# Kernel optimization log

Hardware: AMD Instinct MI355X
Metric: run time of the kernel (lower is better)

## Reference

```python
import jax, jax.numpy as jnp
import numpy as np

VOCAB = 32000
N = 4096        # reservoir_size
D = 32          # avg nonzeros per row -> density D/N
R_OUT = 512
BATCH = 8
T = 256
NNZ = N * D     # W_rec nonzeros = N*N*(D/N)


def setup_inputs() -> dict:
    key = jax.random.key(0)
    ks = jax.random.split(key, 9)
    x = jax.random.randint(ks[0], (BATCH, T), 0, VOCAB)
    # dense input table; sparse.mm(W_in_T, one_hot) == row gather W_in[x_t]
    W_in = jax.random.normal(ks[1], (VOCAB, N), jnp.float32)
    rec_rows = jax.random.randint(ks[2], (NNZ,), 0, N, dtype=jnp.int32)
    rec_cols = jax.random.randint(ks[3], (NNZ,), 0, N, dtype=jnp.int32)
    # small scale stands in for spectral-radius normalization (init-time detail)
    rec_vals = jax.random.normal(ks[4], (NNZ,), jnp.float32) * 0.05
    a = jax.random.uniform(ks[5], (N,), jnp.float32)  # leak rates in [0,1)
    B_w = jax.random.normal(ks[6], (R_OUT, N), jnp.float32) / np.sqrt(N)
    A_w = jax.random.normal(ks[7], (VOCAB, R_OUT), jnp.float32) / np.sqrt(R_OUT)
    A_b = jnp.zeros((VOCAB,), jnp.float32)
    return dict(x=x, W_in=W_in, rec_rows=rec_rows, rec_cols=rec_cols,
                rec_vals=rec_vals, a=a, B_w=B_w, A_w=A_w, A_b=A_b)


def reference(x, W_in, rec_rows, rec_cols, rec_vals, a, B_w, A_w, A_b):
    B = x.shape[0]

    def step(h, x_t):
        # input projection: one-hot @ W_in  ==  row gather
        u = W_in[x_t]                                   # (B, N)
        # sparse COO matvec: rec = W_rec @ h^T, batched over B
        contrib = rec_vals[None, :] * h[:, rec_cols]    # (B, nnz)
        rec = jnp.zeros_like(h).at[:, rec_rows].add(contrib)
        pre = jnp.clip(u + rec, -10.0, 10.0)
        h_new = (1.0 - a) * h + a * jnp.tanh(pre)
        out = (h_new @ B_w.T) @ A_w.T + A_b             # (B, vocab)
        return h_new, out

    h0 = jnp.zeros((B, W_in.shape[1]), W_in.dtype)
    _, outs = jax.lax.scan(step, h0, x.T)               # (T, B, V)
    return jnp.transpose(outs, (1, 0, 2))               # (B, T, V)
```

## Files before the change

kernel.cpp:

```cpp
#include <hip/hip_runtime.h>
#include <hip/hip_bf16.h>
#include <stdint.h>

#define N_RES 4096
#define BATCH 8
#define T_STEPS 256
#define VOCAB 32000
#define R_OUT 512
#define NNZ 131072
#define NNZ_CAP 163840
#define TEAMS 8
#define SLICES 16
#define ROWS_PS 256
#define NWG (TEAMS*SLICES)
#define CSR_CAP 10240

typedef _Float16 v8h __attribute__((ext_vector_type(8)));
typedef float v4f __attribute__((ext_vector_type(4)));

static __device__ __forceinline__ unsigned short f2h(float f) {
    _Float16 h = (_Float16)f;
    unsigned short u;
    __builtin_memcpy(&u, &h, 2);
    return u;
}
static __device__ __forceinline__ float h2f(unsigned short u) {
    _Float16 h;
    __builtin_memcpy(&h, &u, 2);
    return (float)h;
}


#define FLAG_WORDS (TEAMS * SLICES * 32)
#define INIT_WORDS (NNZ_CAP + 4096 + FLAG_WORDS)

__global__ __launch_bounds__(256) void k_init(unsigned* __restrict__ csr,
                                              int* __restrict__ cnt,
                                              unsigned* __restrict__ flags) {
    int i = blockIdx.x * 256 + threadIdx.x;
    if (i < NNZ_CAP) csr[i] = 0u;
    else if (i < NNZ_CAP + 4096) cnt[i - NNZ_CAP] = 0;
    else if (i < INIT_WORDS) flags[i - NNZ_CAP - 4096] = 0u;
}


__global__ __launch_bounds__(256) void k_hist(const int* __restrict__ rows,
                                              int* __restrict__ cnt) {
    int i = blockIdx.x * 256 + threadIdx.x;
    if (i < NNZ) atomicAdd(&cnt[rows[i]], 1);
}

__global__ __launch_bounds__(1024) void k_scan(const int* __restrict__ cnt,
                                               int* __restrict__ row_ptr,
                                               int* __restrict__ cursor) {
    __shared__ int sm[1024];
    int t = threadIdx.x;
    int base = t * 4;
    int c0 = (cnt[base] + 7) & ~7;
    int c1 = (cnt[base + 1] + 7) & ~7;
    int c2 = (cnt[base + 2] + 7) & ~7;
    int c3 = (cnt[base + 3] + 7) & ~7;
    int s = c0 + c1 + c2 + c3;
    sm[t] = s;
    __syncthreads();
    for (int off = 1; off < 1024; off <<= 1) {
        int v = (t >= off) ? sm[t - off] : 0;
        __syncthreads();
        sm[t] += v;
        __syncthreads();
    }
    int run = sm[t] - s;
    row_ptr[base] = run;     cursor[base] = run;     run += c0;
    row_ptr[base + 1] = run; cursor[base + 1] = run; run += c1;
    row_ptr[base + 2] = run; cursor[base + 2] = run; run += c2;
    row_ptr[base + 3] = run; cursor[base + 3] = run; run += c3;
    if (t == 1023) row_ptr[4096] = run;
}

__global__ __launch_bounds__(256) void k_fill(const int* __restrict__ rows,
                                              const int* __restrict__ cols,
                                              const float* __restrict__ vals,
                                              int* __restrict__ cursor,
                                              unsigned* __restrict__ csr) {
    int i = blockIdx.x * 256 + threadIdx.x;
    if (i < NNZ) {
        int r = rows[i];
        int c = cols[i];
        int p = atomicAdd(&cursor[r], 1);
        unsigned off = ((unsigned)(c & 15) << 10) | ((unsigned)(c >> 4) << 2);
        csr[p] = (off << 16) | (unsigned)f2h(vals[i]);
    }
}


#define NB8 (R_OUT * N_RES / 8)
#define NA8 (VOCAB * R_OUT / 8)

__global__ __launch_bounds__(256) void k_cvt2(const float* __restrict__ Bw,
                                              unsigned short* __restrict__ Bwh,
                                              const float* __restrict__ Aw,
                                              unsigned short* __restrict__ Awh) {
    int i = blockIdx.x * 256 + threadIdx.x;
    const float* src;
    unsigned short* dst;
    int j;
    if (i < NB8) { src = Bw; dst = Bwh; j = i * 8; }
    else if (i < NB8 + NA8) { src = Aw; dst = Awh; j = (i - NB8) * 8; }
    else return;
    float4 a0 = *reinterpret_cast<const float4*>(src + j);
    float4 a1 = *reinterpret_cast<const float4*>(src + j + 4);
    unsigned short o[8] = { f2h(a0.x), f2h(a0.y), f2h(a0.z), f2h(a0.w),
                            f2h(a1.x), f2h(a1.y), f2h(a1.z), f2h(a1.w) };
    *reinterpret_cast<uint4*>(dst + j) = *reinterpret_cast<const uint4*>(o);
}


__global__ __launch_bounds__(256) void k_steps(const int* __restrict__ rowptr,
                                               const unsigned* __restrict__ csr,
                                               const float* __restrict__ W_in,
                                               const int* __restrict__ x,
                                               const float* __restrict__ a,
                                               unsigned short* __restrict__ Hb,
                                               unsigned* __restrict__ hx,
                                               unsigned* __restrict__ flags) {
    __shared__ float plane[4096];
    __shared__ __align__(16) unsigned lcsr[CSR_CAP];
    __shared__ int ltok[T_STEPS];

    int wg = blockIdx.x;
    int tid = threadIdx.x;
    int team = wg & 7;
    int slice = wg >> 3;
    int r_own = slice * ROWS_PS + tid;

    ltok[tid] = x[team * T_STEPS + tid];

    int j0 = rowptr[slice * ROWS_PS];
    int j1 = rowptr[slice * ROWS_PS + ROWS_PS];
    int cntE = j1 - j0;
    if (cntE > CSR_CAP) cntE = CSR_CAP;
    {
        const uint4* src = reinterpret_cast<const uint4*>(csr + j0);
        int n4 = cntE >> 2;
        for (int k = tid; k < n4; k += 256)
            reinterpret_cast<uint4*>(lcsr)[k] = src[k];
    }
    for (int k = tid; k < 4096; k += 256) plane[k] = 0.f;

    int js = rowptr[r_own] - j0;
    int je = rowptr[r_own + 1] - j0;
    if (js > CSR_CAP) js = CSR_CAP;
    if (je > CSR_CAP) je = CSR_CAP;
    float av = a[r_own];
    float oma = 1.f - av;
    int pown = ((r_own & 15) << 8) | (r_own >> 4);
    __syncthreads();

    float u_cur = W_in[(size_t)ltok[0] * N_RES + r_own];

    for (int t = 0; t < T_STEPS; ++t) {
        float u_nxt = 0.f;
        if (t + 1 < T_STEPS)
            u_nxt = W_in[(size_t)ltok[t + 1] * N_RES + r_own];

        float acc = 0.f;
        for (int j = js; j < je; j += 8) {
            uint4 e0 = *reinterpret_cast<const uint4*>(lcsr + j);
            uint4 e1 = *reinterpret_cast<const uint4*>(lcsr + j + 4);
            unsigned ee[8] = { e0.x, e0.y, e0.z, e0.w, e1.x, e1.y, e1.z, e1.w };
#pragma unroll
            for (int q = 0; q < 8; ++q) {
                float g = *reinterpret_cast<const float*>(
                    reinterpret_cast<const char*>(plane) + (ee[q] >> 16));
                acc += h2f((unsigned short)(ee[q] & 0xffffu)) * g;
            }
        }
        float hold = plane[pown];
        float pre = u_cur + acc;
        pre = fminf(fmaxf(pre, -10.f), 10.f);
        float ex = __expf(2.f * pre);
        float th = 1.f - 2.f / (ex + 1.f);
        float hv = oma * hold + av * th;
        unsigned short hv16 = f2h(hv);

        if (t == T_STEPS - 1) {
            Hb[((size_t)(team * T_STEPS + t) << 12) + r_own] = hv16;
            break;
        }

        unsigned e = (unsigned)(t + 1);
        unsigned* xb = hx + (((size_t)(e & 1u) * TEAMS + team) << 12);

        __hip_atomic_store(xb + r_own, (e << 16) | (unsigned)hv16,
                           __ATOMIC_RELAXED, __HIP_MEMORY_SCOPE_AGENT);
        __syncthreads();
        if (tid == 0)
            __hip_atomic_store(flags + (team * SLICES + slice) * 32, e,
                               __ATOMIC_RELAXED, __HIP_MEMORY_SCOPE_AGENT);

        Hb[((size_t)(team * T_STEPS + t) << 12) + r_own] = hv16;

        if (tid < SLICES) {
            const unsigned* fp = flags + (team * SLICES + tid) * 32;
            while (__hip_atomic_load(fp, __ATOMIC_RELAXED,
                                     __HIP_MEMORY_SCOPE_AGENT) < e) {}
        }
        __syncthreads();

        uint4 v0, v1, v2, v3;
        const char* p0 = reinterpret_cast<const char*>(xb) + (size_t)tid * 16;
        const char* p1 = p0 + 4096;
        const char* p2 = p0 + 8192;
        const char* p3 = p0 + 12288;
        asm volatile(
            "global_load_dwordx4 %0, %4, off sc0 sc1\n\t"
            "global_load_dwordx4 %1, %5, off sc0 sc1\n\t"
            "global_load_dwordx4 %2, %6, off sc0 sc1\n\t"
            "global_load_dwordx4 %3, %7, off sc0 sc1\n\t"
            "s_waitcnt vmcnt(0)"
            : "=&v"(v0), "=&v"(v1), "=&v"(v2), "=&v"(v3)
            : "v"(p0), "v"(p1), "v"(p2), "v"(p3)
            : "memory");
#define QOK(v) (((v.x >> 16) == e) && ((v.y >> 16) == e) && \
                ((v.z >> 16) == e) && ((v.w >> 16) == e))
        int tries = 0;
        while (!(QOK(v0) && QOK(v1) && QOK(v2) && QOK(v3)) && tries <= 64) {
            ++tries;
            if (!QOK(v0)) asm volatile("global_load_dwordx4 %0, %1, off sc0 sc1\n\ts_waitcnt vmcnt(0)" : "=&v"(v0) : "v"(p0) : "memory");
            if (!QOK(v1)) asm volatile("global_load_dwordx4 %0, %1, off sc0 sc1\n\ts_waitcnt vmcnt(0)" : "=&v"(v1) : "v"(p1) : "memory");
            if (!QOK(v2)) asm volatile("global_load_dwordx4 %0, %1, off sc0 sc1\n\ts_waitcnt vmcnt(0)" : "=&v"(v2) : "v"(p2) : "memory");
            if (!QOK(v3)) asm volatile("global_load_dwordx4 %0, %1, off sc0 sc1\n\ts_waitcnt vmcnt(0)" : "=&v"(v3) : "v"(p3) : "memory");
        }
        if (tries > 64) {
            unsigned w[16];
#pragma unroll
            for (int k = 0; k < 16; ++k) {
                const unsigned* wp = xb + (k >> 2) * 1024 + tid * 4 + (k & 3);
                unsigned g = __hip_atomic_load(wp, __ATOMIC_RELAXED, __HIP_MEMORY_SCOPE_AGENT);
                while ((g >> 16) != e)
                    g = __hip_atomic_load(wp, __ATOMIC_RELAXED, __HIP_MEMORY_SCOPE_AGENT);
                w[k] = g;
            }
            v0 = (uint4){w[0], w[1], w[2], w[3]};
            v1 = (uint4){w[4], w[5], w[6], w[7]};
            v2 = (uint4){w[8], w[9], w[10], w[11]};
            v3 = (uint4){w[12], w[13], w[14], w[15]};
        }
#undef QOK
        {
            unsigned wv[16] = { v0.x, v0.y, v0.z, v0.w, v1.x, v1.y, v1.z, v1.w,
                                v2.x, v2.y, v2.z, v2.w, v3.x, v3.y, v3.z, v3.w };
#pragma unroll
            for (int q = 0; q < 4; ++q)
#pragma unroll
                for (int i = 0; i < 4; ++i) {
                    int r = (q << 10) + 4 * tid + i;
                    plane[((r & 15) << 8) | (r >> 4)] =
                        h2f((unsigned short)(wv[q * 4 + i] & 0xffffu));
                }
        }
        u_cur = u_nxt;
        __syncthreads();
    }
}


static __device__ __forceinline__ void stage128x32(const _Float16* __restrict__ g,
                                                   int ld, int row0, int k0,
                                                   _Float16* lds, int wave, int lane) {
#pragma unroll
    for (int q = 0; q < 2; ++q) {
        int i = wave * 128 + q * 64 + lane;
        const _Float16* src = g + (size_t)(row0 + (i >> 2)) * ld + k0 + (i & 3) * 8;
        int loff = __builtin_amdgcn_readfirstlane((wave * 128 + q * 64) * 16);
        __builtin_amdgcn_global_load_lds(
            (const __attribute__((address_space(1))) void*)src,
            (__attribute__((address_space(3))) void*)((char*)lds + loff),
            16, 0, 0);
    }
}

static __device__ __forceinline__ void stage64x32(const _Float16* __restrict__ g,
                                                  int ld, int row0, int k0,
                                                  _Float16* lds, int wave, int lane) {
    int i = wave * 64 + lane;
    const _Float16* src = g + (size_t)(row0 + (i >> 2)) * ld + k0 + (i & 3) * 8;
    int loff = __builtin_amdgcn_readfirstlane(wave * 64 * 16);
    __builtin_amdgcn_global_load_lds(
        (const __attribute__((address_space(1))) void*)src,
        (__attribute__((address_space(3))) void*)((char*)lds + loff),
        16, 0, 0);
}


__global__ __launch_bounds__(256) void k_gemm1(const _Float16* __restrict__ Hb,
                                               const _Float16* __restrict__ Bwh,
                                               unsigned short* __restrict__ Rbh) {
    __shared__ _Float16 As[2][64 * 32];
    __shared__ _Float16 Bs[2][64 * 32];
    int tid = threadIdx.x, lane = tid & 63, wave = tid >> 6;
    int wm = wave >> 1, wn = wave & 1;
    int col0 = blockIdx.x * 64;
    int row0 = blockIdx.y * 64;
    int rA = lane & 15, kA = (lane >> 4) * 8;
    v4f acc[2][2];
#pragma unroll
    for (int s = 0; s < 2; ++s)
#pragma unroll
        for (int f = 0; f < 2; ++f) acc[s][f] = (v4f){0.f, 0.f, 0.f, 0.f};

    stage64x32(Hb,  N_RES, row0, 0, As[0], wave, lane);
    stage64x32(Bwh, N_RES, col0, 0, Bs[0], wave, lane);
    const int NIT = N_RES / 32;
    for (int it = 0; it < NIT; ++it) {
        int cur = it & 1;
        __syncthreads();
        asm volatile("s_waitcnt vmcnt(0)" ::: "memory");
        __syncthreads();
        if (it + 1 < NIT) {
            stage64x32(Hb,  N_RES, row0, (it + 1) * 32, As[cur ^ 1], wave, lane);
            stage64x32(Bwh, N_RES, col0, (it + 1) * 32, Bs[cur ^ 1], wave, lane);
        }
        v8h af[2], bf[2];
#pragma unroll
        for (int s = 0; s < 2; ++s)
            af[s] = *reinterpret_cast<const v8h*>(&As[cur][(wm * 32 + s * 16 + rA) * 32 + kA]);
#pragma unroll
        for (int f = 0; f < 2; ++f)
            bf[f] = *reinterpret_cast<const v8h*>(&Bs[cur][(wn * 32 + f * 16 + rA) * 32 + kA]);
#pragma unroll
        for (int s = 0; s < 2; ++s)
#pragma unroll
            for (int f = 0; f < 2; ++f)
                acc[s][f] = __builtin_amdgcn_mfma_f32_16x16x32_f16(af[s], bf[f], acc[s][f], 0, 0, 0);
    }
#pragma unroll
    for (int f = 0; f < 2; ++f) {
        int col = col0 + wn * 32 + f * 16 + (lane & 15);
#pragma unroll
        for (int s = 0; s < 2; ++s)
#pragma unroll
            for (int r = 0; r < 2 * 2; ++r) {
                int row = row0 + wm * 32 + s * 16 + (lane >> 4) * 4 + r;
                Rbh[(size_t)row * R_OUT + col] = f2h(acc[s][f][r]);
            }
    }
}


__global__ __launch_bounds__(256) void k_gemm2(const _Float16* __restrict__ Rbh,
                                               const _Float16* __restrict__ Awh,
                                               const float* __restrict__ Ab,
                                               float* __restrict__ out) {
    __shared__ _Float16 As[2][128 * 32];
    __shared__ _Float16 Bs[2][128 * 32];
    int tid = threadIdx.x, lane = tid & 63, wave = tid >> 6;
    int wm = wave >> 1, wn = wave & 1;
    int col0 = blockIdx.x * 128;
    int row0 = blockIdx.y * 128;
    int rA = lane & 15, kA = (lane >> 4) * 8;
    v4f acc[4][4];
#pragma unroll
    for (int s = 0; s < 4; ++s)
#pragma unroll
        for (int f = 0; f < 4; ++f) acc[s][f] = (v4f){0.f, 0.f, 0.f, 0.f};

    stage128x32(Rbh, R_OUT, row0, 0, As[0], wave, lane);
    stage128x32(Awh, R_OUT, col0, 0, Bs[0], wave, lane);
    const int NIT = R_OUT / 32;
    for (int it = 0; it < NIT; ++it) {
        int cur = it & 1;
        __syncthreads();
        asm volatile("s_waitcnt vmcnt(0)" ::: "memory");
        __syncthreads();
        if (it + 1 < NIT) {
            stage128x32(Rbh, R_OUT, row0, (it + 1) * 32, As[cur ^ 1], wave, lane);
            stage128x32(Awh, R_OUT, col0, (it + 1) * 32, Bs[cur ^ 1], wave, lane);
        }
        v8h af[4], bf[4];
#pragma unroll
        for (int s = 0; s < 4; ++s)
            af[s] = *reinterpret_cast<const v8h*>(&As[cur][(wm * 64 + s * 16 + rA) * 32 + kA]);
#pragma unroll
        for (int f = 0; f < 4; ++f)
            bf[f] = *reinterpret_cast<const v8h*>(&Bs[cur][(wn * 64 + f * 16 + rA) * 32 + kA]);
#pragma unroll
        for (int s = 0; s < 4; ++s)
#pragma unroll
            for (int f = 0; f < 4; ++f)
                acc[s][f] = __builtin_amdgcn_mfma_f32_16x16x32_f16(af[s], bf[f], acc[s][f], 0, 0, 0);
    }
#pragma unroll
    for (int f = 0; f < 4; ++f) {
        float bias = Ab[col0 + wn * 64 + f * 16 + (lane & 15)];
#pragma unroll
        for (int s = 0; s < 4; ++s)
#pragma unroll
            for (int r = 0; r < 4; ++r) acc[s][f][r] += bias;
    }
    float* Ct = (float*)As;
#pragma unroll
    for (int s = 0; s < 4; ++s) {
        __syncthreads();
#pragma unroll
        for (int f = 0; f < 4; ++f) {
            int lc = wn * 64 + f * 16 + (lane & 15);
            int lr = wm * 16 + (lane >> 4) * 4;
#pragma unroll
            for (int r = 0; r < 4; ++r)
                Ct[(lr + r) * 128 + lc] = acc[s][f][r];
        }
        __syncthreads();
        int lr2 = tid >> 3;
        int lc2 = (tid & 7) * 16;
        int grow = row0 + (lr2 & 15) + (lr2 >> 4) * 64 + s * 16;
        float* dst = out + (size_t)grow * VOCAB + col0 + lc2;
        const float* srcl = &Ct[lr2 * 128 + lc2];
#pragma unroll
        for (int v = 0; v < 4; ++v)
            *reinterpret_cast<float4*>(dst + v * 4) =
                *reinterpret_cast<const float4*>(srcl + v * 4);
    }
}


extern "C" void kernel_launch(void* const* d_in, const int* in_sizes, int n_in,
                              void* d_out, int out_size, void* d_ws, size_t ws_size,
                              hipStream_t stream) {
    const int*   x        = (const int*)d_in[0];
    const float* W_in     = (const float*)d_in[1];
    const int*   rec_rows = (const int*)d_in[2];
    const int*   rec_cols = (const int*)d_in[3];
    const float* rec_vals = (const float*)d_in[4];
    const float* a        = (const float*)d_in[5];
    const float* B_w      = (const float*)d_in[6];
    const float* A_w      = (const float*)d_in[7];
    const float* A_b      = (const float*)d_in[8];
    float* out = (float*)d_out;

    char* w = (char*)d_ws;
    size_t off = 0;
    auto alloc = [&](size_t bytes) { void* p = w + off; off = (off + bytes + 255) & ~(size_t)255; return p; };

    unsigned short* Hb     = (unsigned short*)alloc((size_t)2048 * N_RES * 2);
    unsigned short* Rbh    = (unsigned short*)alloc((size_t)2048 * R_OUT * 2);
    unsigned short* Bwh    = (unsigned short*)alloc((size_t)R_OUT * N_RES * 2);
    unsigned short* Awh    = (unsigned short*)alloc((size_t)VOCAB * R_OUT * 2);
    unsigned*       csr    = (unsigned*)alloc((size_t)NNZ_CAP * 4);
    int*            rowptr = (int*)alloc(4097 * 4);
    int*            cnt    = (int*)alloc(4096 * 4);
    int*            cursor = (int*)alloc(4096 * 4);
    unsigned*       hx     = (unsigned*)alloc((size_t)2 * TEAMS * 4096 * 4);
    unsigned*       flags  = (unsigned*)alloc(FLAG_WORDS * 4);

    k_init<<<(INIT_WORDS + 255) / 256, 256, 0, stream>>>(csr, cnt, flags);

    k_hist<<<(NNZ + 255) / 256, 256, 0, stream>>>(rec_rows, cnt);
    k_scan<<<1, 1024, 0, stream>>>(cnt, rowptr, cursor);
    k_fill<<<(NNZ + 255) / 256, 256, 0, stream>>>(rec_rows, rec_cols, rec_vals, cursor, csr);

    k_cvt2<<<(NB8 + NA8 + 255) / 256, 256, 0, stream>>>(B_w, Bwh, A_w, Awh);

    k_steps<<<NWG, 256, 0, stream>>>(rowptr, csr, W_in, x, a, Hb, hx, flags);

    k_gemm1<<<dim3(R_OUT / 64, 2048 / 64), 256, 0, stream>>>(
        (const _Float16*)Hb, (const _Float16*)Bwh, Rbh);
    k_gemm2<<<dim3(VOCAB / 128, 2048 / 128), 256, 0, stream>>>(
        (const _Float16*)Rbh, (const _Float16*)Awh, A_b, out);
}
```

Baseline: 1.280 ms.

## Use linear h plane layout, deepen gemm2 K tile, add nontemporal output stores

The recurrent step kernel drops the permuted (r&15,r>>4) plane layout for a linear one. CSR column offsets are now plain byte offsets, and the per-step plane refill becomes four vectorized float4 LDS stores instead of sixteen scattered scalar writes. The output GEMM stages 64-wide K tiles (two 32-wide halves) per iteration, halving the number of barriers and waits, and it writes the large logits output with nontemporal stores. hx is also zeroed in init. A linear layout can bring back LDS bank conflicts on the random gathers, and the larger LDS footprint may reduce gemm2 occupancy.

```diff
diff --git a/kernel.cpp b/kernel.cpp
--- a/kernel.cpp
+++ b/kernel.cpp
@@ -32,15 +32,18 @@
 
 
 #define FLAG_WORDS (TEAMS * SLICES * 32)
-#define INIT_WORDS (NNZ_CAP + 4096 + FLAG_WORDS)
+#define HX_WORDS   (2 * TEAMS * 4096)
+#define INIT_WORDS (NNZ_CAP + 4096 + FLAG_WORDS + HX_WORDS)
 
 __global__ __launch_bounds__(256) void k_init(unsigned* __restrict__ csr,
                                               int* __restrict__ cnt,
-                                              unsigned* __restrict__ flags) {
+                                              unsigned* __restrict__ flags,
+                                              unsigned* __restrict__ hx) {
     int i = blockIdx.x * 256 + threadIdx.x;
     if (i < NNZ_CAP) csr[i] = 0u;
     else if (i < NNZ_CAP + 4096) cnt[i - NNZ_CAP] = 0;
-    else if (i < INIT_WORDS) flags[i - NNZ_CAP - 4096] = 0u;
+    else if (i < NNZ_CAP + 4096 + FLAG_WORDS) flags[i - NNZ_CAP - 4096] = 0u;
+    else if (i < INIT_WORDS) hx[i - NNZ_CAP - 4096 - FLAG_WORDS] = 0u;
 }
 
 
@@ -85,9 +88,8 @@
     int i = blockIdx.x * 256 + threadIdx.x;
     if (i < NNZ) {
         int r = rows[i];
-        int c = cols[i];
+        unsigned off = (unsigned)(cols[i] << 2);
         int p = atomicAdd(&cursor[r], 1);
-        unsigned off = ((unsigned)(c & 15) << 10) | ((unsigned)(c >> 4) << 2);
         csr[p] = (off << 16) | (unsigned)f2h(vals[i]);
     }
 }
@@ -153,7 +155,6 @@
     if (je > CSR_CAP) je = CSR_CAP;
     float av = a[r_own];
     float oma = 1.f - av;
-    int pown = ((r_own & 15) << 8) | (r_own >> 4);
     __syncthreads();
 
     float u_cur = W_in[(size_t)ltok[0] * N_RES + r_own];
@@ -175,7 +176,7 @@
                 acc += h2f((unsigned short)(ee[q] & 0xffffu)) * g;
             }
         }
-        float hold = plane[pown];
+        float hold = plane[r_own];
         float pre = u_cur + acc;
         pre = fminf(fmaxf(pre, -10.f), 10.f);
         float ex = __expf(2.f * pre);
@@ -248,16 +249,16 @@
         }
 #undef QOK
         {
-            unsigned wv[16] = { v0.x, v0.y, v0.z, v0.w, v1.x, v1.y, v1.z, v1.w,
-                                v2.x, v2.y, v2.z, v2.w, v3.x, v3.y, v3.z, v3.w };
-#pragma unroll
-            for (int q = 0; q < 4; ++q)
-#pragma unroll
-                for (int i = 0; i < 4; ++i) {
-                    int r = (q << 10) + 4 * tid + i;
-                    plane[((r & 15) << 8) | (r >> 4)] =
-                        h2f((unsigned short)(wv[q * 4 + i] & 0xffffu));
-                }
+            uint4 qs[4] = { v0, v1, v2, v3 };
+#pragma unroll
+            for (int q = 0; q < 4; ++q) {
+                v4f fv;
+                fv.x = h2f((unsigned short)(qs[q].x & 0xffffu));
+                fv.y = h2f((unsigned short)(qs[q].y & 0xffffu));
+                fv.z = h2f((unsigned short)(qs[q].z & 0xffffu));
+                fv.w = h2f((unsigned short)(qs[q].w & 0xffffu));
+                *reinterpret_cast<v4f*>(&plane[(q << 10) + 4 * tid]) = fv;
+            }
         }
         u_cur = u_nxt;
         __syncthreads();
@@ -340,7 +341,7 @@
 #pragma unroll
         for (int s = 0; s < 2; ++s)
 #pragma unroll
-            for (int r = 0; r < 2 * 2; ++r) {
+            for (int r = 0; r < 4; ++r) {
                 int row = row0 + wm * 32 + s * 16 + (lane >> 4) * 4 + r;
                 Rbh[(size_t)row * R_OUT + col] = f2h(acc[s][f][r]);
             }
@@ -352,8 +353,8 @@
                                                const _Float16* __restrict__ Awh,
                                                const float* __restrict__ Ab,
                                                float* __restrict__ out) {
-    __shared__ _Float16 As[2][128 * 32];
-    __shared__ _Float16 Bs[2][128 * 32];
+    __shared__ _Float16 As[2][128 * 64];
+    __shared__ _Float16 Bs[2][128 * 64];
     int tid = threadIdx.x, lane = tid & 63, wave = tid >> 6;
     int wm = wave >> 1, wn = wave & 1;
     int col0 = blockIdx.x * 128;
@@ -365,30 +366,40 @@
 #pragma unroll
         for (int f = 0; f < 4; ++f) acc[s][f] = (v4f){0.f, 0.f, 0.f, 0.f};
 
-    stage128x32(Rbh, R_OUT, row0, 0, As[0], wave, lane);
-    stage128x32(Awh, R_OUT, col0, 0, Bs[0], wave, lane);
-    const int NIT = R_OUT / 32;
+    stage128x32(Rbh, R_OUT, row0, 0,  As[0], wave, lane);
+    stage128x32(Rbh, R_OUT, row0, 32, As[0] + 128 * 32, wave, lane);
+    stage128x32(Awh, R_OUT, col0, 0,  Bs[0], wave, lane);
+    stage128x32(Awh, R_OUT, col0, 32, Bs[0] + 128 * 32, wave, lane);
+    const int NIT = R_OUT / 64;
     for (int it = 0; it < NIT; ++it) {
         int cur = it & 1;
         __syncthreads();
         asm volatile("s_waitcnt vmcnt(0)" ::: "memory");
         __syncthreads();
         if (it + 1 < NIT) {
-            stage128x32(Rbh, R_OUT, row0, (it + 1) * 32, As[cur ^ 1], wave, lane);
-            stage128x32(Awh, R_OUT, col0, (it + 1) * 32, Bs[cur ^ 1], wave, lane);
-        }
-        v8h af[4], bf[4];
-#pragma unroll
-        for (int s = 0; s < 4; ++s)
-            af[s] = *reinterpret_cast<const v8h*>(&As[cur][(wm * 64 + s * 16 + rA) * 32 + kA]);
-#pragma unroll
-        for (int f = 0; f < 4; ++f)
-            bf[f] = *reinterpret_cast<const v8h*>(&Bs[cur][(wn * 64 + f * 16 + rA) * 32 + kA]);
-#pragma unroll
-        for (int s = 0; s < 4; ++s)
+            int k0 = (it + 1) * 64;
+            stage128x32(Rbh, R_OUT, row0, k0,      As[cur ^ 1], wave, lane);
+            stage128x32(Rbh, R_OUT, row0, k0 + 32, As[cur ^ 1] + 128 * 32, wave, lane);
+            stage128x32(Awh, R_OUT, col0, k0,      Bs[cur ^ 1], wave, lane);
+            stage128x32(Awh, R_OUT, col0, k0 + 32, Bs[cur ^ 1] + 128 * 32, wave, lane);
+        }
+#pragma unroll
+        for (int ks = 0; ks < 2; ++ks) {
+            const _Float16* ab = &As[cur][ks * 128 * 32];
+            const _Float16* bb = &Bs[cur][ks * 128 * 32];
+            v8h af[4], bf[4];
+#pragma unroll
+            for (int s = 0; s < 4; ++s)
+                af[s] = *reinterpret_cast<const v8h*>(&ab[(wm * 64 + s * 16 + rA) * 32 + kA]);
 #pragma unroll
             for (int f = 0; f < 4; ++f)
-                acc[s][f] = __builtin_amdgcn_mfma_f32_16x16x32_f16(af[s], bf[f], acc[s][f], 0, 0, 0);
+                bf[f] = *reinterpret_cast<const v8h*>(&bb[(wn * 64 + f * 16 + rA) * 32 + kA]);
+#pragma unroll
+            for (int s = 0; s < 4; ++s)
+#pragma unroll
+                for (int f = 0; f < 4; ++f)
+                    acc[s][f] = __builtin_amdgcn_mfma_f32_16x16x32_f16(af[s], bf[f], acc[s][f], 0, 0, 0);
+        }
     }
 #pragma unroll
     for (int f = 0; f < 4; ++f) {
@@ -418,8 +429,9 @@
         const float* srcl = &Ct[lr2 * 128 + lc2];
 #pragma unroll
         for (int v = 0; v < 4; ++v)
-            *reinterpret_cast<float4*>(dst + v * 4) =
-                *reinterpret_cast<const float4*>(srcl + v * 4);
+            __builtin_nontemporal_store(
+                *reinterpret_cast<const v4f*>(srcl + v * 4),
+                reinterpret_cast<v4f*>(dst + v * 4));
     }
 }
 
@@ -450,10 +462,10 @@
     int*            rowptr = (int*)alloc(4097 * 4);
     int*            cnt    = (int*)alloc(4096 * 4);
     int*            cursor = (int*)alloc(4096 * 4);
-    unsigned*       hx     = (unsigned*)alloc((size_t)2 * TEAMS * 4096 * 4);
+    unsigned*       hx     = (unsigned*)alloc((size_t)HX_WORDS * 4);
     unsigned*       flags  = (unsigned*)alloc(FLAG_WORDS * 4);
 
-    k_init<<<(INIT_WORDS + 255) / 256, 256, 0, stream>>>(csr, cnt, flags);
+    k_init<<<(INIT_WORDS + 255) / 256, 256, 0, stream>>>(csr, cnt, flags, hx);
 
     k_hist<<<(NNZ + 255) / 256, 256, 0, stream>>>(rec_rows, cnt);
     k_scan<<<1, 1024, 0, stream>>>(cnt, rowptr, cursor);
```

Result: slower. 1.517 ms (+18.5%).
